# Optimization experiments

Measured on AMD Instinct MI355X. Metric: run time of the kernel, lower is better.

The kernel has to match this reference:

```python
import jax, jax.numpy as jnp
import numpy as np

B, N, F_IN, F_OUT = 8, 2048, 128, 128


def setup_inputs() -> dict:
    key = jax.random.key(0)
    k1, k2, k3, k4 = jax.random.split(key, 4)
    h = jax.random.normal(k1, (B, N, F_IN), dtype=jnp.float32)
    adj = (jax.random.uniform(k2, (B, N, N)) > 0.5).astype(jnp.float32)
    adj = jnp.maximum(adj, jnp.eye(N, dtype=jnp.float32)[None])
    # torch nn.Linear weights: W is [out_features, in_features], a is [1, 2*out_features]
    W = jax.random.normal(k3, (F_OUT, F_IN), dtype=jnp.float32) * 0.05
    a = jax.random.normal(k4, (1, 2 * F_OUT), dtype=jnp.float32) * 0.05
    return {"h": h, "adj": adj, "W": W, "a": a}


def reference(h, adj, W, a):
    # Wh = W(h): [B, N, F_OUT]
    Wh = jnp.einsum("bnf,of->bno", h, W)
    # attn_fc(concat(Wh_i, Wh_j)) == (Wh_i @ a1) + (Wh_j @ a2): exact split of the
    # linear layer, avoiding the O(B*N*N*2F) concat intermediate.
    a1 = a[0, :F_OUT]
    a2 = a[0, F_OUT:]
    e_i = Wh @ a1  # [B, N]  score contribution of destination node i
    e_j = Wh @ a2  # [B, N]  score contribution of source node j
    e = e_i[:, :, None] + e_j[:, None, :]  # [B, N, N]
    e = e + (1.0 - adj) * (-1e9)
    alpha = jax.nn.softmax(e, axis=-1)  # [B, N, N]
    # weighted aggregation: h_out[b,i] = sum_j alpha[b,i,j] * Wh[b,j]
    h_out = jnp.einsum("bij,bjo->bio", alpha, Wh)
    return h_out
```

## Files before the change

kernel.cpp:

```cpp
#include <hip/hip_runtime.h>
#include <stdint.h>

#define AS1 __attribute__((address_space(1)))
#define AS3 __attribute__((address_space(3)))

typedef __bf16 bf16x8 __attribute__((ext_vector_type(8)));
typedef float f32x4 __attribute__((ext_vector_type(4)));
typedef unsigned int u32x4 __attribute__((ext_vector_type(4)));

constexpr int NB = 8;
constexpr int N  = 2048;
constexpr int F  = 128;

__device__ __forceinline__ unsigned short bf16r(float f) {
    unsigned u = __float_as_uint(f);
    return (unsigned short)((u + 0x7FFFu + ((u >> 16) & 1u)) >> 16);
}
__device__ __forceinline__ float bf2f(unsigned short s) {
    return __uint_as_float(((unsigned)s) << 16);
}


__global__ __launch_bounds__(256) void k01_wh(const float* __restrict__ h,
                                              const float* __restrict__ adj,
                                              const float* __restrict__ W,
                                              const float* __restrict__ a,
                                              unsigned short* __restrict__ Wb2,
                                              unsigned short* __restrict__ p16,
                                              unsigned char* __restrict__ maskG) {
    const int tid  = threadIdx.x;
    const int lane = tid & 63, wid = tid >> 6;

    if (blockIdx.x >= 256) {
        const int cid = blockIdx.x - 256;
#pragma unroll
        for (int rr = 0; rr < 2; ++rr) {
            const int row = cid * 8 + wid * 2 + rr;
            const float2* src = (const float2*)(adj + (size_t)row * 2048) + lane;
            u32x4* dst = (u32x4*)(maskG + (size_t)row * 256);
#pragma unroll 4
            for (int t = 0; t < 16; ++t) {
                float2 v = src[t * 64];
                unsigned long long m0 = __ballot(v.x > 0.5f);
                unsigned long long m1 = __ballot(v.y > 0.5f);
                if (lane == 0) {
                    u32x4 w = { (unsigned)m0, (unsigned)(m0 >> 32),
                                (unsigned)m1, (unsigned)(m1 >> 32) };
                    dst[t] = w;
                }
            }
        }
        return;
    }

    __shared__ float epart[2][64];

    const int quad = lane >> 4, l15 = lane & 15;
    const int wm = wid >> 1, wn = wid & 1;
    const int m0 = blockIdx.x * 64;
    const int batch = m0 >> 11;
    const int nbase = m0 & 2047;

    f32x4 acc[2][4] = {};

#pragma unroll
    for (int kk = 0; kk < 4; ++kk) {
        const int k = kk * 32 + quad * 8;
        bf16x8 afr[2], bfr[4];
#pragma unroll
        for (int rt = 0; rt < 2; ++rt) {
            const float* src = h + (size_t)(m0 + wm * 32 + rt * 16 + l15) * F + k;
            float4 x0 = *(const float4*)src;
            float4 x1 = *(const float4*)(src + 4);
            afr[rt][0] = (__bf16)x0.x; afr[rt][1] = (__bf16)x0.y;
            afr[rt][2] = (__bf16)x0.z; afr[rt][3] = (__bf16)x0.w;
            afr[rt][4] = (__bf16)x1.x; afr[rt][5] = (__bf16)x1.y;
            afr[rt][6] = (__bf16)x1.z; afr[rt][7] = (__bf16)x1.w;
        }
#pragma unroll
        for (int ct = 0; ct < 4; ++ct) {
            const int o = wn * 64 + ct * 16 + l15;
            const float* src = W + (size_t)o * F + k;
            float4 x0 = *(const float4*)src;
            float4 x1 = *(const float4*)(src + 4);
            bfr[ct][0] = (__bf16)x0.x; bfr[ct][1] = (__bf16)x0.y;
            bfr[ct][2] = (__bf16)x0.z; bfr[ct][3] = (__bf16)x0.w;
            bfr[ct][4] = (__bf16)x1.x; bfr[ct][5] = (__bf16)x1.y;
            bfr[ct][6] = (__bf16)x1.z; bfr[ct][7] = (__bf16)x1.w;
        }
#pragma unroll
        for (int rt = 0; rt < 2; ++rt)
#pragma unroll
            for (int ct = 0; ct < 4; ++ct)
                acc[rt][ct] = __builtin_amdgcn_mfma_f32_16x16x32_bf16(
                    afr[rt], bfr[ct], acc[rt][ct], 0, 0, 0);
    }

    float a2v[4];
#pragma unroll
    for (int ct = 0; ct < 4; ++ct) a2v[ct] = a[F + wn * 64 + ct * 16 + l15];

    float ep[2][4];
#pragma unroll
    for (int rt = 0; rt < 2; ++rt)
#pragma unroll
        for (int g = 0; g < 4; ++g) {
            float s = 0.f;
#pragma unroll
            for (int ct = 0; ct < 4; ++ct) s += acc[rt][ct][g] * a2v[ct];
            ep[rt][g] = s;
        }
#pragma unroll
    for (int m = 1; m < 16; m <<= 1)
#pragma unroll
        for (int rt = 0; rt < 2; ++rt)
#pragma unroll
            for (int g = 0; g < 4; ++g)
                ep[rt][g] += __shfl_xor(ep[rt][g], m);

    if (l15 == 0)
#pragma unroll
        for (int rt = 0; rt < 2; ++rt)
#pragma unroll
            for (int g = 0; g < 4; ++g)
                epart[wn][wm * 32 + rt * 16 + quad * 4 + g] = ep[rt][g];
    __syncthreads();

#pragma unroll
    for (int rt = 0; rt < 2; ++rt)
#pragma unroll
        for (int ct = 0; ct < 4; ++ct) {
            const int o  = wn * 64 + ct * 16 + l15;
            const int r0 = wm * 32 + rt * 16 + quad * 4;
            const int n0 = nbase + r0;
            ushort4 v;
#pragma unroll
            for (int g = 0; g < 4; ++g) {
                const float e  = epart[0][r0 + g] + epart[1][r0 + g];
                const float pf = bf2f(bf16r(expf(e)));
                (&v.x)[g] = bf16r(pf * acc[rt][ct][g]);
            }
            size_t off = (size_t)batch * N * F + (size_t)(n0 >> 3) * 1024 + o * 8 + (n0 & 7);
            *(ushort4*)&Wb2[off] = v;
        }

    if (tid < 64) {
        const float e = epart[0][tid] + epart[1][tid];
        p16[batch * N + nbase + tid] = bf16r(expf(e));
    }
}

__global__ __launch_bounds__(256, 2) void k3_fused(const unsigned char* __restrict__ maskG,
                                                   const unsigned short* __restrict__ Wb2,
                                                   const unsigned short* __restrict__ p16,
                                                   float* __restrict__ out) {
    const int tid  = threadIdx.x;
    const int lane = tid & 63, wid = tid >> 6;
    const int quad = lane >> 4, l15 = lane & 15;
    const int b  = blockIdx.x & 7;
    const int it = blockIdx.x >> 3;
    const int i0 = it * 32;

    const u32x4* mrow0 = (const u32x4*)(maskG + (size_t)(b * 2048 + i0 + l15) * 256);
    const u32x4* mrow1 = (const u32x4*)(maskG + (size_t)(b * 2048 + i0 + 16 + l15) * 256);
    const char* wb = (const char*)Wb2 + (size_t)b * (N * F * 2)
                   + quad * 2048 + (wid * 32 + l15) * 16;
    const char* pp = (const char*)p16 + (size_t)b * N * 2 + quad * 16;

    f32x4 acc[2][2] = {};
    f32x4 dacc[2] = {};

#pragma unroll 2
    for (int t = 0; t < 16; ++t) {
        const u32x4 q0 = mrow0[t];
        const u32x4 q1 = mrow1[t];
#pragma unroll
        for (int s = 0; s < 4; ++s) {
            const int j0 = t * 128 + s * 32;
            const char* bc = wb + (size_t)j0 * 256;
            bf16x8 bf0 = *(const bf16x8*)(bc);
            bf16x8 bf1 = *(const bf16x8*)(bc + 256);
            bf16x8 pv  = *(const bf16x8*)(pp + j0 * 2);

            const unsigned uE0 = (s >> 1) ? q0.y : q0.x;
            const unsigned uO0 = (s >> 1) ? q0.w : q0.z;
            const unsigned uE1 = (s >> 1) ? q1.y : q1.x;
            const unsigned uO1 = (s >> 1) ? q1.w : q1.z;
            const int base = (s & 1) * 16 + quad * 4;
            u32x4 aw0, aw1;
#pragma unroll
            for (int i = 0; i < 4; ++i) {
                const int bi = base + i;
                aw0[i] = (((uE0 >> bi) & 1u) ? 0x00003F80u : 0u)
                       | (((uO0 >> bi) & 1u) ? 0x3F800000u : 0u);
                aw1[i] = (((uE1 >> bi) & 1u) ? 0x00003F80u : 0u)
                       | (((uO1 >> bi) & 1u) ? 0x3F800000u : 0u);
            }
            bf16x8 af0 = __builtin_bit_cast(bf16x8, aw0);
            bf16x8 af1 = __builtin_bit_cast(bf16x8, aw1);

            acc[0][0] = __builtin_amdgcn_mfma_f32_16x16x32_bf16(af0, bf0, acc[0][0], 0, 0, 0);
            acc[0][1] = __builtin_amdgcn_mfma_f32_16x16x32_bf16(af0, bf1, acc[0][1], 0, 0, 0);
            acc[1][0] = __builtin_amdgcn_mfma_f32_16x16x32_bf16(af1, bf0, acc[1][0], 0, 0, 0);
            acc[1][1] = __builtin_amdgcn_mfma_f32_16x16x32_bf16(af1, bf1, acc[1][1], 0, 0, 0);
            dacc[0]   = __builtin_amdgcn_mfma_f32_16x16x32_bf16(af0, pv,  dacc[0],  0, 0, 0);
            dacc[1]   = __builtin_amdgcn_mfma_f32_16x16x32_bf16(af1, pv,  dacc[1],  0, 0, 0);
        }
    }

#pragma unroll
    for (int rt = 0; rt < 2; ++rt)
#pragma unroll
        for (int g = 0; g < 4; ++g) {
            const float inv = 1.0f / dacc[rt][g];
            float* orow = out + ((size_t)b * N + i0 + rt * 16 + quad * 4 + g) * F
                        + wid * 32 + l15;
            orow[0]  = acc[rt][0][g] * inv;
            orow[16] = acc[rt][1][g] * inv;
        }
}

extern "C" void kernel_launch(void* const* d_in, const int* in_sizes, int n_in,
                              void* d_out, int out_size, void* d_ws, size_t ws_size,
                              hipStream_t stream) {
    const float* h   = (const float*)d_in[0];
    const float* adj = (const float*)d_in[1];
    const float* W   = (const float*)d_in[2];
    const float* a   = (const float*)d_in[3];
    float* out = (float*)d_out;

    unsigned short* Wb2   = (unsigned short*)d_ws;
    unsigned short* p16   = (unsigned short*)((char*)d_ws + (4u << 20));
    unsigned char*  maskG = (unsigned char*)((char*)d_ws + (8u << 20));

    k01_wh<<<256 + 2048, 256, 0, stream>>>(h, adj, W, a, Wb2, p16, maskG);
    k3_fused<<<NB * 64, 256, 0, stream>>>(maskG, Wb2, p16, out);
}
```

Baseline: 240.6 us.

## Split attention aggregation over source-node chunks with LDS-staged tiles and reduction kernel

Replaces the per-32-row fused aggregation kernel with a split-K scheme. Each 512-thread block handles 256 destination rows against one eighth of the source nodes, staging Wh tiles into LDS through a triple-buffered global_load_lds pipeline so loads are reused across many rows. Partial numerators (bf16) and denominators go to a workspace, and a new reduce kernel sums them and normalises. This aims to cut redundant global reads of Wh, at the cost of an extra launch, extra workspace traffic, and bf16 rounding of the partial sums.

```diff
diff --git a/kernel.cpp b/kernel.cpp
--- a/kernel.cpp
+++ b/kernel.cpp
@@ -11,6 +11,8 @@
 constexpr int NB = 8;
 constexpr int N  = 2048;
 constexpr int F  = 128;
+constexpr size_t NSL = (size_t)NB * N * F;
+constexpr size_t DSL = (size_t)NB * N;
 
 __device__ __forceinline__ unsigned short bf16r(float f) {
     unsigned u = __float_as_uint(f);
@@ -150,74 +152,140 @@
     }
 }
 
-__global__ __launch_bounds__(256, 2) void k3_fused(const unsigned char* __restrict__ maskG,
-                                                   const unsigned short* __restrict__ Wb2,
-                                                   const unsigned short* __restrict__ p16,
-                                                   float* __restrict__ out) {
+__global__ __launch_bounds__(512, 2) void k3_attn(const unsigned char* __restrict__ maskG,
+                                                  const unsigned short* __restrict__ Wb2,
+                                                  const unsigned short* __restrict__ p16,
+                                                  unsigned short* __restrict__ nump,
+                                                  float* __restrict__ denp) {
+    __shared__ __align__(16) char  Bsm_[3][8192];
+    __shared__ __align__(16) u32x4 Msm_[2][256];
+    __shared__ __align__(16) char  Psm_[512];
+
     const int tid  = threadIdx.x;
     const int lane = tid & 63, wid = tid >> 6;
     const int quad = lane >> 4, l15 = lane & 15;
+    const int wr = wid >> 1, wn = wid & 1;
     const int b  = blockIdx.x & 7;
-    const int it = blockIdx.x >> 3;
-    const int i0 = it * 32;
-
-    const u32x4* mrow0 = (const u32x4*)(maskG + (size_t)(b * 2048 + i0 + l15) * 256);
-    const u32x4* mrow1 = (const u32x4*)(maskG + (size_t)(b * 2048 + i0 + 16 + l15) * 256);
-    const char* wb = (const char*)Wb2 + (size_t)b * (N * F * 2)
-                   + quad * 2048 + (wid * 32 + l15) * 16;
-    const char* pp = (const char*)p16 + (size_t)b * N * 2 + quad * 16;
-
-    f32x4 acc[2][2] = {};
-    f32x4 dacc[2] = {};
-
-#pragma unroll 2
-    for (int t = 0; t < 16; ++t) {
-        const u32x4 q0 = mrow0[t];
-        const u32x4 q1 = mrow1[t];
-#pragma unroll
-        for (int s = 0; s < 4; ++s) {
-            const int j0 = t * 128 + s * 32;
-            const char* bc = wb + (size_t)j0 * 256;
-            bf16x8 bf0 = *(const bf16x8*)(bc);
-            bf16x8 bf1 = *(const bf16x8*)(bc + 256);
-            bf16x8 pv  = *(const bf16x8*)(pp + j0 * 2);
-
-            const unsigned uE0 = (s >> 1) ? q0.y : q0.x;
-            const unsigned uO0 = (s >> 1) ? q0.w : q0.z;
-            const unsigned uE1 = (s >> 1) ? q1.y : q1.x;
-            const unsigned uO1 = (s >> 1) ? q1.w : q1.z;
-            const int base = (s & 1) * 16 + quad * 4;
-            u32x4 aw0, aw1;
-#pragma unroll
-            for (int i = 0; i < 4; ++i) {
-                const int bi = base + i;
-                aw0[i] = (((uE0 >> bi) & 1u) ? 0x00003F80u : 0u)
-                       | (((uO0 >> bi) & 1u) ? 0x3F800000u : 0u);
-                aw1[i] = (((uE1 >> bi) & 1u) ? 0x00003F80u : 0u)
-                       | (((uO1 >> bi) & 1u) ? 0x3F800000u : 0u);
+    const int r  = blockIdx.x >> 3;
+    const int it = r >> 3, jq = r & 7;
+    const int i0 = it * 256;
+
+    const int mr = tid >> 1, ms = tid & 1;
+    u32x4 mv = *(const u32x4*)(maskG + (size_t)(b * 2048 + i0 + mr) * 256
+                               + (size_t)(2 * jq + ms) * 16);
+    u32x4 pvv = {};
+    if (tid < 32)
+        pvv = *(const u32x4*)((const char*)p16 + (size_t)b * N * 2 + jq * 512 + tid * 16);
+    Msm_[ms][mr] = mv;
+    if (tid < 32) *(u32x4*)&Psm_[tid * 16] = pvv;
+
+    const char* bSrc = (const char*)Wb2 + (size_t)b * (N * F * 2)
+                     + (size_t)jq * 65536 + wid * 1024 + lane * 16;
+
+#define K3_STAGE(BI, C)                                                            \
+    __builtin_amdgcn_global_load_lds(                                              \
+        (const AS1 void*)(bSrc + (size_t)(C) * 8192),                              \
+        (AS3 void*)(&Bsm_[BI][wid * 1024]), 16, 0, 0);
+
+    f32x4 acc[4][4] = {};
+    f32x4 dacc[4] = {};
+
+    K3_STAGE(0, 0)
+    K3_STAGE(1, 1)
+    K3_STAGE(2, 2)
+    __syncthreads();
+
+#define K3_CHUNK(C, BI, WAITSTR, DOSTAGE)                                          \
+    {                                                                              \
+        asm volatile(WAITSTR ::: "memory");                                        \
+        __builtin_amdgcn_s_barrier();                                              \
+        __builtin_amdgcn_sched_barrier(0);                                         \
+        const char* bB = &Bsm_[BI][0];                                             \
+        bf16x8 pv = *(const bf16x8*)(&Psm_[(C) * 64 + quad * 16]);                 \
+        bf16x8 bfv[4];                                                             \
+        _Pragma("unroll")                                                          \
+        for (int ct = 0; ct < 4; ++ct)                                             \
+            bfv[ct] = *(const bf16x8*)(bB + quad * 2048                            \
+                          + (wn * 64 + ct * 16 + l15) * 16);                       \
+        _Pragma("unroll")                                                          \
+        for (int rt = 0; rt < 4; ++rt) {                                           \
+            const int row = wr * 64 + rt * 16 + l15;                               \
+            u32x4 q = Msm_[(C) >> 2][row];                                         \
+            const unsigned uE = ((C) & 2) ? q.y : q.x;                             \
+            const unsigned uO = ((C) & 2) ? q.w : q.z;                             \
+            const int base = ((C) & 1) * 16 + quad * 4;                            \
+            u32x4 aw;                                                              \
+            _Pragma("unroll")                                                      \
+            for (int i = 0; i < 4; ++i) {                                          \
+                const int bi_ = base + i;                                          \
+                aw[i] = (((uE >> bi_) & 1u) ? 0x00003F80u : 0u)                    \
+                      | (((uO >> bi_) & 1u) ? 0x3F800000u : 0u);                   \
+            }                                                                      \
+            bf16x8 af = __builtin_bit_cast(bf16x8, aw);                            \
+            _Pragma("unroll")                                                      \
+            for (int ct = 0; ct < 4; ++ct)                                         \
+                acc[rt][ct] = __builtin_amdgcn_mfma_f32_16x16x32_bf16(             \
+                    af, bfv[ct], acc[rt][ct], 0, 0, 0);                            \
+            dacc[rt] = __builtin_amdgcn_mfma_f32_16x16x32_bf16(                    \
+                af, pv, dacc[rt], 0, 0, 0);                                        \
+        }                                                                          \
+        if (DOSTAGE) {                                                             \
+            __builtin_amdgcn_s_barrier();                                          \
+            __builtin_amdgcn_sched_barrier(0);                                     \
+            K3_STAGE(BI, (C) + 3)                                                  \
+        }                                                                          \
+    }
+
+    K3_CHUNK(0, 0, "s_waitcnt vmcnt(2)", 1)
+    K3_CHUNK(1, 1, "s_waitcnt vmcnt(2)", 1)
+    K3_CHUNK(2, 2, "s_waitcnt vmcnt(2)", 1)
+    K3_CHUNK(3, 0, "s_waitcnt vmcnt(2)", 1)
+    K3_CHUNK(4, 1, "s_waitcnt vmcnt(2)", 1)
+    K3_CHUNK(5, 2, "s_waitcnt vmcnt(2)", 0)
+    K3_CHUNK(6, 0, "s_waitcnt vmcnt(1)", 0)
+    K3_CHUNK(7, 1, "s_waitcnt vmcnt(0)", 0)
+
+#undef K3_CHUNK
+#undef K3_STAGE
+
+    unsigned short* np = nump + (size_t)jq * NSL + (size_t)b * N * F;
+    float* dp = denp + (size_t)jq * DSL + (size_t)b * N;
+#pragma unroll
+    for (int rt = 0; rt < 4; ++rt) {
+#pragma unroll
+        for (int ct = 0; ct < 4; ++ct) {
+            const int o = wn * 64 + ct * 16 + l15;
+#pragma unroll
+            for (int g = 0; g < 4; ++g) {
+                const int i = i0 + wr * 64 + rt * 16 + quad * 4 + g;
+                np[(size_t)i * F + o] = bf16r(acc[rt][ct][g]);
             }
-            bf16x8 af0 = __builtin_bit_cast(bf16x8, aw0);
-            bf16x8 af1 = __builtin_bit_cast(bf16x8, aw1);
-
-            acc[0][0] = __builtin_amdgcn_mfma_f32_16x16x32_bf16(af0, bf0, acc[0][0], 0, 0, 0);
-            acc[0][1] = __builtin_amdgcn_mfma_f32_16x16x32_bf16(af0, bf1, acc[0][1], 0, 0, 0);
-            acc[1][0] = __builtin_amdgcn_mfma_f32_16x16x32_bf16(af1, bf0, acc[1][0], 0, 0, 0);
-            acc[1][1] = __builtin_amdgcn_mfma_f32_16x16x32_bf16(af1, bf1, acc[1][1], 0, 0, 0);
-            dacc[0]   = __builtin_amdgcn_mfma_f32_16x16x32_bf16(af0, pv,  dacc[0],  0, 0, 0);
-            dacc[1]   = __builtin_amdgcn_mfma_f32_16x16x32_bf16(af1, pv,  dacc[1],  0, 0, 0);
-        }
-    }
-
-#pragma unroll
-    for (int rt = 0; rt < 2; ++rt)
-#pragma unroll
-        for (int g = 0; g < 4; ++g) {
-            const float inv = 1.0f / dacc[rt][g];
-            float* orow = out + ((size_t)b * N + i0 + rt * 16 + quad * 4 + g) * F
-                        + wid * 32 + l15;
-            orow[0]  = acc[rt][0][g] * inv;
-            orow[16] = acc[rt][1][g] * inv;
-        }
+        }
+        if (l15 == 0)
+#pragma unroll
+            for (int g = 0; g < 4; ++g)
+                dp[i0 + wr * 64 + rt * 16 + quad * 4 + g] = dacc[rt][g];
+    }
+}
+
+__global__ __launch_bounds__(256) void k4_reduce(const unsigned short* __restrict__ nump,
+                                                 const float* __restrict__ denp,
+                                                 float* __restrict__ out) {
+    const int b   = blockIdx.x & 7;
+    const int row = (blockIdx.x >> 3) * 8 + (threadIdx.x >> 5);
+    const int o4  = (threadIdx.x & 31) * 4;
+    const size_t base = ((size_t)b * N + row) * F + o4;
+
+    float s0 = 0.f, s1 = 0.f, s2 = 0.f, s3 = 0.f, d = 0.f;
+#pragma unroll
+    for (int q = 0; q < 8; ++q) {
+        ushort4 v = *(const ushort4*)&nump[q * NSL + base];
+        s0 += bf2f(v.x); s1 += bf2f(v.y); s2 += bf2f(v.z); s3 += bf2f(v.w);
+        d  += denp[q * DSL + (size_t)b * N + row];
+    }
+    const float inv = 1.0f / d;
+    f32x4 o = { s0 * inv, s1 * inv, s2 * inv, s3 * inv };
+    *(f32x4*)&out[base] = o;
 }
 
 extern "C" void kernel_launch(void* const* d_in, const int* in_sizes, int n_in,
@@ -232,7 +300,10 @@
     unsigned short* Wb2   = (unsigned short*)d_ws;
     unsigned short* p16   = (unsigned short*)((char*)d_ws + (4u << 20));
     unsigned char*  maskG = (unsigned char*)((char*)d_ws + (8u << 20));
+    unsigned short* nump  = (unsigned short*)((char*)d_ws + (16u << 20));
+    float*          denp  = (float*)((char*)d_ws + (48u << 20));
 
     k01_wh<<<256 + 2048, 256, 0, stream>>>(h, adj, W, a, Wb2, p16, maskG);
-    k3_fused<<<NB * 64, 256, 0, stream>>>(maskG, Wb2, p16, out);
-}
+    k3_attn<<<NB * 64, 512, 0, stream>>>(maskG, Wb2, p16, nump, denp);
+    k4_reduce<<<NB * N / 8, 256, 0, stream>>>(nump, denp, out);
+}
```

New measurement: 239.9 us. No clear change (-0.3%).
